# Optimization experiments

Measured on AMD Instinct MI355X. Metric: run time of the kernel, lower is better.

## Reference

```python
import jax, jax.numpy as jnp
import numpy as np

THETA = 10.0
TOP_K = 12
EPS = 1e-8  # torch F.cosine_similarity eps


def setup_inputs() -> dict:
    key = jax.random.key(0)
    h = jax.random.normal(key, (8192, 512), dtype=jnp.float32)
    return {"h": h}


def reference(h):
    # cosine similarity: normalize with clamped norm like torch (eps=1e-8)
    norm = jnp.linalg.norm(h, axis=-1, keepdims=True)
    hn = h / jnp.maximum(norm, EPS)
    # Sim[i, j] = cos(h[i], h[j]); [N, N]
    Sim = jnp.einsum('id,jd->ij', hn, hn)
    # top-k neighbors per row
    sim_topk, idx_topk = jax.lax.top_k(Sim, TOP_K)          # [N, k]
    beta = jax.nn.softmax(THETA * sim_topk, axis=-1)        # [N, k]
    h_topk = h[idx_topk]                                    # [N, k, d]
    # dropout is identity in eval mode
    h_sim = jnp.einsum('nk,nkd->nd', beta, h_topk)          # [N, d]
    return h_sim
```

## Files before the change

### kernel.cpp

```cpp
#include <hip/hip_runtime.h>
#include <hip/hip_bf16.h>

#define N 8192
#define D 512
#define K_TOP 12
#define THETA 10.0f
#define EPS 1e-8f
#define TAU 0.10f
#define CAPL 6
#define CAPG 192
#define NPAIR 2080
#define NBLK 1024
#define INVQ2 (1.0f / 16129.0f)

typedef int i32x4 __attribute__((ext_vector_type(4)));
typedef int i32x16 __attribute__((ext_vector_type(16)));

__device__ __forceinline__ unsigned int bf16_bits_rne(float v) {
    unsigned int u = __float_as_uint(v);
    u += 0x7FFFu + ((u >> 16) & 1u);
    return u >> 16;
}

__device__ __forceinline__ int sb(unsigned int u, int idx) {
    return ((int)(u << (24 - 8 * idx))) >> 24;
}

__device__ __forceinline__ void load16(const unsigned char* g, unsigned char* l) {
    __builtin_amdgcn_global_load_lds(
        (const __attribute__((address_space(1))) unsigned int*)g,
        (__attribute__((address_space(3))) unsigned int*)l, 16, 0, 0);
}

__device__ __forceinline__ void decode_pair(int p, int& it, int& jt) {
    int j = (int)((sqrtf(8.0f * (float)p + 1.0f) - 1.0f) * 0.5f);
    while ((j + 1) * (j + 2) / 2 <= p) ++j;
    while (j * (j + 1) / 2 > p) --j;
    jt = j;
    it = p - j * (j + 1) / 2;
}

__global__ __launch_bounds__(256) void norm_kernel(const float* __restrict__ h,
                                                   unsigned char* __restrict__ hq,
                                                   float* __restrict__ norms,
                                                   int* __restrict__ gcnt,
                                                   int* __restrict__ gflag) {
    int row = blockIdx.x * 4 + (threadIdx.x >> 6);
    int lane = threadIdx.x & 63;
    const float4* hr4 = (const float4*)(h + (size_t)row * D);
    float4 p0 = hr4[lane], p1 = hr4[64 + lane];
    float ss = p0.x * p0.x + p0.y * p0.y + p0.z * p0.z + p0.w * p0.w +
               p1.x * p1.x + p1.y * p1.y + p1.z * p1.z + p1.w * p1.w;
#pragma unroll
    for (int off = 32; off > 0; off >>= 1) ss += __shfl_xor(ss, off, 64);
    float nrm = fmaxf(sqrtf(ss), EPS);
    float inv = 127.0f / nrm;
    if (lane == 0) { gcnt[row] = 0; gflag[row] = 0; norms[row] = nrm; }
    int a0 = __float2int_rn(p0.x * inv), a1 = __float2int_rn(p0.y * inv);
    int a2 = __float2int_rn(p0.z * inv), a3 = __float2int_rn(p0.w * inv);
    int b0 = __float2int_rn(p1.x * inv), b1 = __float2int_rn(p1.y * inv);
    int b2 = __float2int_rn(p1.z * inv), b3 = __float2int_rn(p1.w * inv);
    unsigned int w0 = (a0 & 255) | ((a1 & 255) << 8) | ((a2 & 255) << 16) | ((a3 & 255) << 24);
    unsigned int w1 = (b0 & 255) | ((b1 & 255) << 8) | ((b2 & 255) << 16) | ((b3 & 255) << 24);
    unsigned int* q32 = (unsigned int*)(hq + (size_t)row * D);
    q32[lane] = w0;
    q32[64 + lane] = w1;
}

__global__ __launch_bounds__(256, 4) void simfp8_kernel(
        const unsigned char* __restrict__ hq,
        unsigned int* __restrict__ gcand,
        int* __restrict__ gcnt,
        int* __restrict__ gflag) {
    __shared__ unsigned char tiles[2][2][128 * 64];
    __shared__ int cnt[256];
    __shared__ unsigned int lbuf[256][CAPL];

    const int b = blockIdx.x;
    const int t = threadIdx.x;
    const int wave = t >> 6, lane = t & 63;
    const int wr = (wave >> 1) * 64, wc = (wave & 1) * 64;
    const int lm32 = lane & 31, lg2 = lane >> 5;
    const int rk = (lm32 >> 2) & 3;

    const int srow = t >> 2;
    const int sq = (t & 3) ^ ((t >> 4) & 3);

    const int i0s = (32 + (b >> 1)) * 128;
    const int j0s = 63 * 128 + (b & 1) * 64;
    const bool sdiag = ((b >> 1) == 31);

    cnt[t] = 0;

    auto issue = [&](int ii0, int jj0, int r_) {
        int sel = r_ & 1;
        const unsigned char* gA = hq + (size_t)(ii0 + srow) * D + r_ * 64 + sq * 16;
        const unsigned char* gB = hq + (size_t)(jj0 + srow) * D + r_ * 64 + sq * 16;
        unsigned char* lA = &tiles[sel][0][t * 16];
        unsigned char* lB = &tiles[sel][1][t * 16];
#pragma unroll
        for (int e = 0; e < 2; e++) {
            load16(gA + (size_t)(e * 64) * D, lA + e * 4096);
            load16(gB + (size_t)(e * 64) * D, lB + e * 4096);
        }
    };

    auto issue_strip = [&](int r_) {
        int sel = r_ & 1;
        const unsigned char* gA = hq + (size_t)(i0s + srow) * D + r_ * 64 + sq * 16;
        const unsigned char* gB = hq + (size_t)(j0s + srow) * D + r_ * 64 + sq * 16;
        unsigned char* lA = &tiles[sel][0][t * 16];
#pragma unroll
        for (int e = 0; e < 2; e++)
            load16(gA + (size_t)(e * 64) * D, lA + e * 4096);
        load16(gB, &tiles[sel][1][t * 16]);
    };

    int cit, cjt;
    decode_pair(b, cit, cjt);
    int ci0 = cit * 128, cj0 = cjt * 128;
    bool cdiag = (cit == cjt);
    int ni0 = 0, nj0 = 0;
    bool ndiag = false;
    {
        int nit, njt;
        decode_pair(b + NBLK, nit, njt);
        ni0 = nit * 128; nj0 = njt * 128; ndiag = (nit == njt);
    }
    issue(ci0, cj0, 0);

    i32x16 acc[2][2];
#pragma unroll
    for (int x = 0; x < 2; x++)
#pragma unroll
        for (int y = 0; y < 2; y++)
#pragma unroll
            for (int q = 0; q < 16; q++) acc[x][y][q] = 0;

    for (int qp = 0; qp < 2; qp++) {
        for (int r = 0; r < 8; r++) {
            const int sel = r & 1;

            __builtin_amdgcn_s_barrier();
            if (r < 7) {
                issue(ci0, cj0, r + 1);
                asm volatile("s_waitcnt vmcnt(4)" ::: "memory");
            } else if (qp == 0) {
                issue(ni0, nj0, 0);
                asm volatile("s_waitcnt vmcnt(4)" ::: "memory");
            } else if (b < 64) {
                issue_strip(0);
                asm volatile("s_waitcnt vmcnt(3)" ::: "memory");
            } else {
                asm volatile("s_waitcnt vmcnt(0)" ::: "memory");
            }
            __builtin_amdgcn_s_barrier();

#pragma unroll
            for (int kk = 0; kk < 2; kk++) {
                const int kb = (((kk << 1) | lg2) ^ rk) << 4;
                i32x4 af[2], bfr[2];
#pragma unroll
                for (int x = 0; x < 2; x++)
                    af[x] = *(const i32x4*)&tiles[sel][0][(wr + x * 32 + lm32) * 64 + kb];
#pragma unroll
                for (int y = 0; y < 2; y++)
                    bfr[y] = *(const i32x4*)&tiles[sel][1][(wc + y * 32 + lm32) * 64 + kb];
#pragma unroll
                for (int x = 0; x < 2; x++)
#pragma unroll
                    for (int y = 0; y < 2; y++)
                        acc[x][y] = __builtin_amdgcn_mfma_i32_32x32x32_i8(
                            af[x], bfr[y], acc[x][y], 0, 0, 0);
            }
        }

#pragma unroll
        for (int x = 0; x < 2; x++)
#pragma unroll
            for (int y = 0; y < 2; y++) {
                int lcol = wc + y * 32 + lm32;
                int gcol = cj0 + lcol;
#pragma unroll
                for (int q = 0; q < 16; q++) {
                    int rr = wr + x * 32 + (q & 3) + 8 * (q >> 2) + 4 * lg2;
                    int gi = ci0 + rr;
                    float v = (float)acc[x][y][q] * INVQ2;
                    acc[x][y][q] = 0;
                    if (gi == gcol) v = 1.0f;
                    if (v > TAU) {
                        unsigned int vb = bf16_bits_rne(v) << 16;
                        int idx = atomicAdd(&cnt[rr], 1);
                        if (idx < CAPL) lbuf[rr][idx] = vb | (unsigned int)gcol;
                        else {
                            int pg = atomicAdd(&gcnt[gi], 1);
                            if (pg < CAPG) gcand[(size_t)gi * CAPG + pg] = vb | (unsigned int)gcol;
                            else gflag[gi] = 1;
                        }
                        if (!cdiag) {
                            int idx2 = atomicAdd(&cnt[128 + lcol], 1);
                            if (idx2 < CAPL) lbuf[128 + lcol][idx2] = vb | (unsigned int)gi;
                            else {
                                int pg = atomicAdd(&gcnt[gcol], 1);
                                if (pg < CAPG) gcand[(size_t)gcol * CAPG + pg] = vb | (unsigned int)gi;
                                else gflag[gcol] = 1;
                            }
                        }
                    }
                }
            }

        __syncthreads();
        {
            int grow = (t < 128) ? (ci0 + t) : (cj0 + t - 128);
            int c = cnt[t];
            int s = c < CAPL ? c : CAPL;
            if (s > 0) {
                int base = atomicAdd(&gcnt[grow], s);
                unsigned int* dst = gcand + (size_t)grow * CAPG;
                for (int k = 0; k < s; k++) {
                    int pp = base + k;
                    if (pp < CAPG) dst[pp] = lbuf[t][k];
                    else gflag[grow] = 1;
                }
            }
            cnt[t] = 0;
        }

        ci0 = ni0; cj0 = nj0; cdiag = ndiag;
    }

    if (b >= 64) return;

    {
        const int wr2 = wave * 32;
        i32x16 sacc[2];
#pragma unroll
        for (int y = 0; y < 2; y++)
#pragma unroll
            for (int q = 0; q < 16; q++) sacc[y][q] = 0;

        for (int r = 0; r < 8; r++) {
            const int sel = r & 1;

            __builtin_amdgcn_s_barrier();
            if (r < 7) {
                issue_strip(r + 1);
                asm volatile("s_waitcnt vmcnt(3)" ::: "memory");
            } else {
                asm volatile("s_waitcnt vmcnt(0)" ::: "memory");
            }
            __builtin_amdgcn_s_barrier();

#pragma unroll
            for (int kk = 0; kk < 2; kk++) {
                const int kb = (((kk << 1) | lg2) ^ rk) << 4;
                i32x4 af = *(const i32x4*)&tiles[sel][0][(wr2 + lm32) * 64 + kb];
                i32x4 bfr[2];
#pragma unroll
                for (int y = 0; y < 2; y++)
                    bfr[y] = *(const i32x4*)&tiles[sel][1][(y * 32 + lm32) * 64 + kb];
#pragma unroll
                for (int y = 0; y < 2; y++)
                    sacc[y] = __builtin_amdgcn_mfma_i32_32x32x32_i8(
                        af, bfr[y], sacc[y], 0, 0, 0);
            }
        }

#pragma unroll
        for (int y = 0; y < 2; y++) {
            int lcol = y * 32 + lm32;
            int gcol = j0s + lcol;
#pragma unroll
            for (int q = 0; q < 16; q++) {
                int rr = wr2 + (q & 3) + 8 * (q >> 2) + 4 * lg2;
                int gi = i0s + rr;
                float v = (float)sacc[y][q] * INVQ2;
                if (gi == gcol) v = 1.0f;
                if (v > TAU) {
                    unsigned int vb = bf16_bits_rne(v) << 16;
                    int idx = atomicAdd(&cnt[rr], 1);
                    if (idx < CAPL) lbuf[rr][idx] = vb | (unsigned int)gcol;
                    else {
                        int pg = atomicAdd(&gcnt[gi], 1);
                        if (pg < CAPG) gcand[(size_t)gi * CAPG + pg] = vb | (unsigned int)gcol;
                        else gflag[gi] = 1;
                    }
                    if (!sdiag) {
                        int idx2 = atomicAdd(&cnt[128 + lcol], 1);
                        if (idx2 < CAPL) lbuf[128 + lcol][idx2] = vb | (unsigned int)gi;
                        else {
                            int pg = atomicAdd(&gcnt[gcol], 1);
                            if (pg < CAPG) gcand[(size_t)gcol * CAPG + pg] = vb | (unsigned int)gi;
                            else gflag[gcol] = 1;
                        }
                    }
                }
            }
        }

        __syncthreads();
        if (t < 192) {
            int grow = (t < 128) ? (i0s + t) : (j0s + t - 128);
            int c = cnt[t];
            int s = c < CAPL ? c : CAPL;
            if (s > 0) {
                int base = atomicAdd(&gcnt[grow], s);
                unsigned int* dst = gcand + (size_t)grow * CAPG;
                for (int k = 0; k < s; k++) {
                    int pp = base + k;
                    if (pp < CAPG) dst[pp] = lbuf[t][k];
                    else gflag[grow] = 1;
                }
            }
        }
    }
}

__global__ __launch_bounds__(256) void gather_kernel(const float* __restrict__ h,
                                                     const unsigned char* __restrict__ hq,
                                                     const float* __restrict__ norms,
                                                     const unsigned int* __restrict__ gcand,
                                                     const int* __restrict__ gcnt,
                                                     const int* __restrict__ gflag,
                                                     float* __restrict__ out) {
    int row = blockIdx.x * 4 + (threadIdx.x >> 6);
    int lane = threadIdx.x & 63;

    const float4* hr4 = (const float4*)(h + (size_t)row * D);
    float4 s0 = hr4[lane], s1 = hr4[64 + lane];

    int c = gcnt[row];

    float selv[K_TOP];
    int selj[K_TOP];

    if (c >= K_TOP && c <= CAPG && gflag[row] == 0) {
        const unsigned int* cr = gcand + (size_t)row * CAPG;
        unsigned int e[3];
#pragma unroll
        for (int q = 0; q < 3; q++) {
            int idx = lane + 64 * q;
            e[q] = (idx < c) ? cr[idx] : 0u;
        }
#pragma unroll
        for (int k = 0; k < K_TOP; k++) {
            unsigned int m = e[0];
            if (e[1] > m) m = e[1];
            if (e[2] > m) m = e[2];
#pragma unroll
            for (int off = 32; off > 0; off >>= 1) {
                unsigned int om = __shfl_xor(m, off, 64);
                if (om > m) m = om;
            }
            selv[k] = __uint_as_float(m & 0xFFFF0000u);
            selj[k] = (int)(m & 0x1FFFu);
#pragma unroll
            for (int q = 0; q < 3; q++)
                if (e[q] == m) e[q] = 0u;
        }
    } else {
        float vals[K_TOP];
        int idxs[K_TOP];
#pragma unroll
        for (int q = 0; q < K_TOP; q++) { vals[q] = -3e38f; idxs[q] = 0; }
        float minv = -3e38f;
        int minp = 0;
        const unsigned int* rp = (const unsigned int*)(hq + (size_t)row * D);
        for (int col = lane; col < N; col += 64) {
            const unsigned int* cp = (const unsigned int*)(hq + (size_t)col * D);
            int isum = 0;
            for (int k4 = 0; k4 < D / 4; k4++) {
                unsigned int ra = rp[k4], ca = cp[k4];
                isum += sb(ra, 0) * sb(ca, 0) + sb(ra, 1) * sb(ca, 1) +
                        sb(ra, 2) * sb(ca, 2) + sb(ra, 3) * sb(ca, 3);
            }
            float s = (float)isum * INVQ2;
            if (col == row) s = 1.0f;
            if (s > minv) {
                vals[minp] = s; idxs[minp] = col;
                minv = vals[0]; minp = 0;
#pragma unroll
                for (int q = 1; q < K_TOP; q++)
                    if (vals[q] < minv) { minv = vals[q]; minp = q; }
            }
        }
        for (int k = 0; k < K_TOP; k++) {
            float bv = vals[0]; int bp = 0;
#pragma unroll
            for (int q = 1; q < K_TOP; q++)
                if (vals[q] > bv) { bv = vals[q]; bp = q; }
            float v = bv; int j = idxs[bp]; int src = lane;
#pragma unroll
            for (int off = 32; off > 0; off >>= 1) {
                float ov = __shfl_xor(v, off, 64);
                int oj = __shfl_xor(j, off, 64);
                int os = __shfl_xor(src, off, 64);
                if (ov > v || (ov == v && os < src)) { v = ov; j = oj; src = os; }
            }
            selv[k] = __uint_as_float((unsigned int)(bf16_bits_rne(v) << 16));
            selj[k] = j;
            if (lane == src) vals[bp] = -3e38f;
        }
    }

    unsigned int na[K_TOP], nb[K_TOP];
    float wn[K_TOP];
#pragma unroll
    for (int q = 0; q < K_TOP; q++) {
        const unsigned int* r32 = (const unsigned int*)(hq + (size_t)selj[q] * D);
        na[q] = r32[lane];
        nb[q] = r32[64 + lane];
        wn[q] = norms[selj[q]];
    }

    float mx = selv[0];
    float beta[K_TOP];
    float sum = 0.f;
#pragma unroll
    for (int q = 0; q < K_TOP; q++) { beta[q] = __expf(THETA * (selv[q] - mx)); sum += beta[q]; }
    float rs = 1.0f / sum;

    float acc[8];
#pragma unroll
    for (int ee = 0; ee < 8; ee++) acc[ee] = 0.f;
#pragma unroll
    for (int q = 0; q < K_TOP; q++) {
        float w = beta[q] * rs;
        if (selj[q] == row) {
            acc[0] += w * s0.x; acc[1] += w * s0.y; acc[2] += w * s0.z; acc[3] += w * s0.w;
            acc[4] += w * s1.x; acc[5] += w * s1.y; acc[6] += w * s1.z; acc[7] += w * s1.w;
        } else {
            float wj = w * wn[q] * (1.0f / 127.0f);
            acc[0] += wj * (float)sb(na[q], 0);
            acc[1] += wj * (float)sb(na[q], 1);
            acc[2] += wj * (float)sb(na[q], 2);
            acc[3] += wj * (float)sb(na[q], 3);
            acc[4] += wj * (float)sb(nb[q], 0);
            acc[5] += wj * (float)sb(nb[q], 1);
            acc[6] += wj * (float)sb(nb[q], 2);
            acc[7] += wj * (float)sb(nb[q], 3);
        }
    }
    float4* o4 = (float4*)(out + (size_t)row * D);
    o4[lane] = make_float4(acc[0], acc[1], acc[2], acc[3]);
    o4[64 + lane] = make_float4(acc[4], acc[5], acc[6], acc[7]);
}

extern "C" void kernel_launch(void* const* d_in, const int* in_sizes, int n_in,
                              void* d_out, int out_size, void* d_ws, size_t ws_size,
                              hipStream_t stream) {
    const float* h = (const float*)d_in[0];
    float* out = (float*)d_out;

    char* ws = (char*)d_ws;
    unsigned char* hq = (unsigned char*)ws;
    size_t off = (size_t)N * D;
    float* norms = (float*)(ws + off);
    int* gcnt = (int*)(ws + off + (size_t)N * 4);
    int* gflag = (int*)(ws + off + (size_t)N * 8);
    unsigned int* gcand = (unsigned int*)(ws + off + (size_t)N * 12);

    norm_kernel<<<N / 4, 256, 0, stream>>>(h, hq, norms, gcnt, gflag);
    simfp8_kernel<<<NBLK, 256, 0, stream>>>(hq, gcand, gcnt, gflag);
    gather_kernel<<<N / 4, 256, 0, stream>>>(h, hq, norms, gcand, gcnt, gflag, out);
}
```

Before: 126.3 us.

## Pack two tile pairs per 512-thread block in int8 similarity kernel

```diff
diff --git a/kernel.cpp b/kernel.cpp
--- a/kernel.cpp
+++ b/kernel.cpp
@@ -10,7 +10,7 @@
 #define CAPL 6
 #define CAPG 192
 #define NPAIR 2080
-#define NBLK 1024
+#define NBLK2 512
 #define INVQ2 (1.0f / 16129.0f)
 
 typedef int i32x4 __attribute__((ext_vector_type(4)));
@@ -67,28 +67,27 @@
     q32[64 + lane] = w1;
 }
 
-__global__ __launch_bounds__(256, 4) void simfp8_kernel(
+__global__ __launch_bounds__(512, 4) void simfp8_kernel(
         const unsigned char* __restrict__ hq,
         unsigned int* __restrict__ gcand,
         int* __restrict__ gcnt,
         int* __restrict__ gflag) {
-    __shared__ unsigned char tiles[2][2][128 * 64];
-    __shared__ int cnt[256];
-    __shared__ unsigned int lbuf[256][CAPL];
+    __shared__ unsigned char tiles[2][2][2][128 * 64];
+    __shared__ int cnt[512];
+    __shared__ unsigned int lbuf[512][CAPL];
 
     const int b = blockIdx.x;
     const int t = threadIdx.x;
     const int wave = t >> 6, lane = t & 63;
-    const int wr = (wave >> 1) * 64, wc = (wave & 1) * 64;
+    const int pw = wave >> 2;
+    const int sw = wave & 3;
+    const int wr = (sw >> 1) * 64, wc = (sw & 1) * 64;
     const int lm32 = lane & 31, lg2 = lane >> 5;
     const int rk = (lm32 >> 2) & 3;
 
-    const int srow = t >> 2;
-    const int sq = (t & 3) ^ ((t >> 4) & 3);
-
-    const int i0s = (32 + (b >> 1)) * 128;
-    const int j0s = 63 * 128 + (b & 1) * 64;
-    const bool sdiag = ((b >> 1) == 31);
+    const int tt = t & 255;
+    const int srow = tt >> 2;
+    const int sq = (tt & 3) ^ ((tt >> 4) & 3);
 
     cnt[t] = 0;
 
@@ -96,8 +95,8 @@
         int sel = r_ & 1;
         const unsigned char* gA = hq + (size_t)(ii0 + srow) * D + r_ * 64 + sq * 16;
         const unsigned char* gB = hq + (size_t)(jj0 + srow) * D + r_ * 64 + sq * 16;
-        unsigned char* lA = &tiles[sel][0][t * 16];
-        unsigned char* lB = &tiles[sel][1][t * 16];
+        unsigned char* lA = &tiles[sel][pw][0][tt * 16];
+        unsigned char* lB = &tiles[sel][pw][1][tt * 16];
 #pragma unroll
         for (int e = 0; e < 2; e++) {
             load16(gA + (size_t)(e * 64) * D, lA + e * 4096);
@@ -105,29 +104,30 @@
         }
     };
 
+    const int i0s = (32 + (b >> 1)) * 128;
+    const int j0s = 63 * 128 + (b & 1) * 64;
+    const bool sdiag = ((b >> 1) == 31);
+    const int sarow = t >> 2;
+    const int saq = (t & 3) ^ ((t >> 4) & 3);
     auto issue_strip = [&](int r_) {
         int sel = r_ & 1;
-        const unsigned char* gA = hq + (size_t)(i0s + srow) * D + r_ * 64 + sq * 16;
-        const unsigned char* gB = hq + (size_t)(j0s + srow) * D + r_ * 64 + sq * 16;
-        unsigned char* lA = &tiles[sel][0][t * 16];
-#pragma unroll
-        for (int e = 0; e < 2; e++)
-            load16(gA + (size_t)(e * 64) * D, lA + e * 4096);
-        load16(gB, &tiles[sel][1][t * 16]);
+        const unsigned char* gA = hq + (size_t)(i0s + sarow) * D + r_ * 64 + saq * 16;
+        load16(gA, &tiles[sel][0][0][t * 16]);
+        if (t < 256) {
+            const unsigned char* gB = hq + (size_t)(j0s + srow) * D + r_ * 64 + sq * 16;
+            load16(gB, &tiles[sel][0][1][tt * 16]);
+        }
     };
 
-    int cit, cjt;
-    decode_pair(b, cit, cjt);
-    int ci0 = cit * 128, cj0 = cjt * 128;
-    bool cdiag = (cit == cjt);
-    int ni0 = 0, nj0 = 0;
-    bool ndiag = false;
-    {
-        int nit, njt;
-        decode_pair(b + NBLK, nit, njt);
-        ni0 = nit * 128; nj0 = njt * 128; ndiag = (nit == njt);
-    }
-    issue(ci0, cj0, 0);
+    int ia, ja, ib, jb;
+    decode_pair(2 * b, ia, ja);
+    decode_pair(2 * b + 1, ib, jb);
+    int i0a = ia * 128, j0a = ja * 128, i0b = ib * 128, j0b = jb * 128;
+    bool dga = (ia == ja), dgb = (ib == jb);
+
+    int my_i0 = pw ? i0b : i0a, my_j0 = pw ? j0b : j0a;
+    bool my_dg = pw ? dgb : dga;
+    issue(my_i0, my_j0, 0);
 
     i32x16 acc[2][2];
 #pragma unroll
@@ -138,19 +138,27 @@
             for (int q = 0; q < 16; q++) acc[x][y][q] = 0;
 
     for (int qp = 0; qp < 2; qp++) {
+        int n_i0 = 0, n_j0 = 0;
+        if (qp == 0) {
+            int i2, j2;
+            decode_pair(2 * b + pw + 1024, i2, j2);
+            n_i0 = i2 * 128; n_j0 = j2 * 128;
+        }
+
         for (int r = 0; r < 8; r++) {
             const int sel = r & 1;
 
             __builtin_amdgcn_s_barrier();
             if (r < 7) {
-                issue(ci0, cj0, r + 1);
+                issue(my_i0, my_j0, r + 1);
                 asm volatile("s_waitcnt vmcnt(4)" ::: "memory");
             } else if (qp == 0) {
-                issue(ni0, nj0, 0);
+                issue(n_i0, n_j0, 0);
                 asm volatile("s_waitcnt vmcnt(4)" ::: "memory");
             } else if (b < 64) {
                 issue_strip(0);
-                asm volatile("s_waitcnt vmcnt(3)" ::: "memory");
+                if (wave < 4) { asm volatile("s_waitcnt vmcnt(2)" ::: "memory"); }
+                else          { asm volatile("s_waitcnt vmcnt(1)" ::: "memory"); }
             } else {
                 asm volatile("s_waitcnt vmcnt(0)" ::: "memory");
             }
@@ -162,10 +170,10 @@
                 i32x4 af[2], bfr[2];
 #pragma unroll
                 for (int x = 0; x < 2; x++)
-                    af[x] = *(const i32x4*)&tiles[sel][0][(wr + x * 32 + lm32) * 64 + kb];
+                    af[x] = *(const i32x4*)&tiles[sel][pw][0][(wr + x * 32 + lm32) * 64 + kb];
 #pragma unroll
                 for (int y = 0; y < 2; y++)
-                    bfr[y] = *(const i32x4*)&tiles[sel][1][(wc + y * 32 + lm32) * 64 + kb];
+                    bfr[y] = *(const i32x4*)&tiles[sel][pw][1][(wc + y * 32 + lm32) * 64 + kb];
 #pragma unroll
                 for (int x = 0; x < 2; x++)
 #pragma unroll
@@ -175,31 +183,32 @@
             }
         }
 
+        const int cbase = pw * 256;
 #pragma unroll
         for (int x = 0; x < 2; x++)
 #pragma unroll
             for (int y = 0; y < 2; y++) {
                 int lcol = wc + y * 32 + lm32;
-                int gcol = cj0 + lcol;
+                int gcol = my_j0 + lcol;
 #pragma unroll
                 for (int q = 0; q < 16; q++) {
                     int rr = wr + x * 32 + (q & 3) + 8 * (q >> 2) + 4 * lg2;
-                    int gi = ci0 + rr;
+                    int gi = my_i0 + rr;
                     float v = (float)acc[x][y][q] * INVQ2;
                     acc[x][y][q] = 0;
                     if (gi == gcol) v = 1.0f;
                     if (v > TAU) {
                         unsigned int vb = bf16_bits_rne(v) << 16;
-                        int idx = atomicAdd(&cnt[rr], 1);
-                        if (idx < CAPL) lbuf[rr][idx] = vb | (unsigned int)gcol;
+                        int idx = atomicAdd(&cnt[cbase + rr], 1);
+                        if (idx < CAPL) lbuf[cbase + rr][idx] = vb | (unsigned int)gcol;
                         else {
                             int pg = atomicAdd(&gcnt[gi], 1);
                             if (pg < CAPG) gcand[(size_t)gi * CAPG + pg] = vb | (unsigned int)gcol;
                             else gflag[gi] = 1;
                         }
-                        if (!cdiag) {
-                            int idx2 = atomicAdd(&cnt[128 + lcol], 1);
-                            if (idx2 < CAPL) lbuf[128 + lcol][idx2] = vb | (unsigned int)gi;
+                        if (!my_dg) {
+                            int idx2 = atomicAdd(&cnt[cbase + 128 + lcol], 1);
+                            if (idx2 < CAPL) lbuf[cbase + 128 + lcol][idx2] = vb | (unsigned int)gi;
                             else {
                                 int pg = atomicAdd(&gcnt[gcol], 1);
                                 if (pg < CAPG) gcand[(size_t)gcol * CAPG + pg] = vb | (unsigned int)gi;
@@ -212,7 +221,9 @@
 
         __syncthreads();
         {
-            int grow = (t < 128) ? (ci0 + t) : (cj0 + t - 128);
+            int p2 = t >> 8, idx = t & 255;
+            int p_i0 = p2 ? i0b : i0a, p_j0 = p2 ? j0b : j0a;
+            int grow = (idx < 128) ? (p_i0 + idx) : (p_j0 + idx - 128);
             int c = cnt[t];
             int s = c < CAPL ? c : CAPL;
             if (s > 0) {
@@ -227,18 +238,23 @@
             cnt[t] = 0;
         }
 
-        ci0 = ni0; cj0 = nj0; cdiag = ndiag;
+        if (qp == 0) {
+            decode_pair(2 * b + 1024, ia, ja);
+            decode_pair(2 * b + 1025, ib, jb);
+            i0a = ia * 128; j0a = ja * 128; i0b = ib * 128; j0b = jb * 128;
+            dga = (ia == ja); dgb = (ib == jb);
+            my_i0 = pw ? i0b : i0a; my_j0 = pw ? j0b : j0a;
+            my_dg = pw ? dgb : dga;
+        }
     }
 
     if (b >= 64) return;
 
     {
-        const int wr2 = wave * 32;
-        i32x16 sacc[2];
-#pragma unroll
-        for (int y = 0; y < 2; y++)
-#pragma unroll
-            for (int q = 0; q < 16; q++) sacc[y][q] = 0;
+        const int wr2 = (wave >> 1) * 32, wc2 = (wave & 1) * 32;
+        i32x16 sacc;
+#pragma unroll
+        for (int q = 0; q < 16; q++) sacc[q] = 0;
 
         for (int r = 0; r < 8; r++) {
             const int sel = r & 1;
@@ -246,7 +262,8 @@
             __builtin_amdgcn_s_barrier();
             if (r < 7) {
                 issue_strip(r + 1);
-                asm volatile("s_waitcnt vmcnt(3)" ::: "memory");
+                if (wave < 4) { asm volatile("s_waitcnt vmcnt(2)" ::: "memory"); }
+                else          { asm volatile("s_waitcnt vmcnt(1)" ::: "memory"); }
             } else {
                 asm volatile("s_waitcnt vmcnt(0)" ::: "memory");
             }
@@ -255,27 +272,20 @@
 #pragma unroll
             for (int kk = 0; kk < 2; kk++) {
                 const int kb = (((kk << 1) | lg2) ^ rk) << 4;
-                i32x4 af = *(const i32x4*)&tiles[sel][0][(wr2 + lm32) * 64 + kb];
-                i32x4 bfr[2];
-#pragma unroll
-                for (int y = 0; y < 2; y++)
-                    bfr[y] = *(const i32x4*)&tiles[sel][1][(y * 32 + lm32) * 64 + kb];
-#pragma unroll
-                for (int y = 0; y < 2; y++)
-                    sacc[y] = __builtin_amdgcn_mfma_i32_32x32x32_i8(
-                        af, bfr[y], sacc[y], 0, 0, 0);
-            }
-        }
-
-#pragma unroll
-        for (int y = 0; y < 2; y++) {
-            int lcol = y * 32 + lm32;
+                i32x4 af = *(const i32x4*)&tiles[sel][0][0][(wr2 + lm32) * 64 + kb];
+                i32x4 bfr = *(const i32x4*)&tiles[sel][0][1][(wc2 + lm32) * 64 + kb];
+                sacc = __builtin_amdgcn_mfma_i32_32x32x32_i8(af, bfr, sacc, 0, 0, 0);
+            }
+        }
+
+        {
+            int lcol = wc2 + lm32;
             int gcol = j0s + lcol;
 #pragma unroll
             for (int q = 0; q < 16; q++) {
                 int rr = wr2 + (q & 3) + 8 * (q >> 2) + 4 * lg2;
                 int gi = i0s + rr;
-                float v = (float)sacc[y][q] * INVQ2;
+                float v = (float)sacc[q] * INVQ2;
                 if (gi == gcol) v = 1.0f;
                 if (v > TAU) {
                     unsigned int vb = bf16_bits_rne(v) << 16;
@@ -462,6 +472,6 @@
     unsigned int* gcand = (unsigned int*)(ws + off + (size_t)N * 12);
 
     norm_kernel<<<N / 4, 256, 0, stream>>>(h, hq, norms, gcnt, gflag);
-    simfp8_kernel<<<NBLK, 256, 0, stream>>>(hq, gcand, gcnt, gflag);
+    simfp8_kernel<<<NBLK2, 512, 0, stream>>>(hq, gcand, gcnt, gflag);
     gather_kernel<<<N / 4, 256, 0, stream>>>(h, hq, norms, gcand, gcnt, gflag, out);
 }
```

Result: slower. 150.2 us (+18.9%).
